# Optimization experiments

Measured on AMD Instinct MI355X. Metric: run time of the kernel, lower is better.

The kernel has to match this reference:

```python
import jax, jax.numpy as jnp
import numpy as np
from jax import lax

B = 1048576
H = 4  # hidden size of both RNN cells


def setup_inputs() -> dict:
    key = jax.random.key(0)
    ks = jax.random.split(key, 16)
    s = 0.3  # small init scale, keeps tanh out of deep saturation
    return {
        "x": jax.random.normal(ks[0], (B, 18), dtype=jnp.float32),
        # r_up = nn.RNNCell(2, 4)
        "Wih_up": jax.random.normal(ks[1], (H, 2), dtype=jnp.float32) * s,
        "Whh_up": jax.random.normal(ks[2], (H, H), dtype=jnp.float32) * s,
        "bih_up": jax.random.normal(ks[3], (H,), dtype=jnp.float32) * s,
        "bhh_up": jax.random.normal(ks[4], (H,), dtype=jnp.float32) * s,
        # fc_obs_1 = nn.Linear(8, 4)
        "W1": jax.random.normal(ks[5], (H, 8), dtype=jnp.float32) * s,
        "b1": jax.random.normal(ks[6], (H,), dtype=jnp.float32) * s,
        # fc_obs_2 = nn.Linear(4, 4)
        "W2": jax.random.normal(ks[7], (H, H), dtype=jnp.float32) * s,
        "b2": jax.random.normal(ks[8], (H,), dtype=jnp.float32) * s,
        # r_down = nn.RNNCell(4, 4)
        "Wih_dn": jax.random.normal(ks[9], (H, H), dtype=jnp.float32) * s,
        "Whh_dn": jax.random.normal(ks[10], (H, H), dtype=jnp.float32) * s,
        "bih_dn": jax.random.normal(ks[11], (H,), dtype=jnp.float32) * s,
        "bhh_dn": jax.random.normal(ks[12], (H,), dtype=jnp.float32) * s,
        # fc_out = nn.Linear(5, 1)
        "Wo": jax.random.normal(ks[13], (1, 5), dtype=jnp.float32) * s,
        "bo": jax.random.normal(ks[14], (1,), dtype=jnp.float32) * s,
    }


def reference(x, Wih_up, Whh_up, bih_up, bhh_up, W1, b1, W2, b2,
              Wih_dn, Whh_dn, bih_dn, bhh_dn, Wo, bo):
    b = x.shape[0]
    obs = x[:, :4]            # [B,4]
    j = x[:, 4:11]            # [B,7] joint angles
    jd = x[:, 11:18]          # [B,7] joint velocities

    # --- upward recurrence: i = 6 .. 0 over joints ---
    seq_up = jnp.stack([j.T, jd.T], axis=-1)[::-1]  # [7,B,2], step order 6..0

    def up_step(h, inp):
        h_new = jnp.tanh(inp @ Wih_up.T + bih_up + h @ Whh_up.T + bhh_up)
        return h_new, h_new

    h_last, h_up_rev = lax.scan(up_step, jnp.zeros((b, H), x.dtype), seq_up)
    h_up = h_up_rev[::-1]  # h_up[i] = hidden after consuming joint i (loop ran 6..0)

    # --- obs MLP ---
    h0 = jnp.tanh(jnp.concatenate([obs, h_last], axis=1) @ W1.T + b1)
    h0 = jnp.tanh(h0 @ W2.T + b2)  # [B,4]

    # --- downward recurrence: i = 0 .. 6, action uses pre-update hidden ---
    def down_step(h, xs):
        hu, ji = xs  # hu: [B,4], ji: [B,1]
        act = jnp.concatenate([h, ji], axis=1) @ Wo.T + bo  # uses h_prev
        h_new = jnp.tanh(hu @ Wih_dn.T + bih_dn + h @ Whh_dn.T + bhh_dn)
        return h_new, act

    _, acts = lax.scan(down_step, h0, (h_up, j.T[:, :, None]))  # acts: [7,B,1]
    return acts[:, :, 0].T  # [B,7]
```

## Files before the change

kernel.cpp:

```cpp
#include <hip/hip_runtime.h>

#define ROWS 256

__device__ __forceinline__ float uni(float v) {
    return __int_as_float(__builtin_amdgcn_readfirstlane(__float_as_int(v)));
}

__device__ __forceinline__ float fast_tanh(float x) {
    float e = __builtin_amdgcn_exp2f(x * 2.885390081777927f);
    float r = __builtin_amdgcn_rcpf(e + 1.0f);
    return fmaf(-2.0f, r, 1.0f);
}

__global__ __launch_bounds__(ROWS)
void recpolicy_kernel(const float* __restrict__ x,
                      const float* __restrict__ Wih_up,
                      const float* __restrict__ Whh_up,
                      const float* __restrict__ bih_up,
                      const float* __restrict__ bhh_up,
                      const float* __restrict__ W1,
                      const float* __restrict__ b1,
                      const float* __restrict__ W2,
                      const float* __restrict__ b2,
                      const float* __restrict__ Wih_dn,
                      const float* __restrict__ Whh_dn,
                      const float* __restrict__ bih_dn,
                      const float* __restrict__ bhh_dn,
                      const float* __restrict__ Wo,
                      const float* __restrict__ bo,
                      float* __restrict__ out)
{
    __shared__ float xs[ROWS * 19];
    const int tid = threadIdx.x;
    const long long row0 = (long long)blockIdx.x * ROWS;

    const float2* xg2 = (const float2*)(x + row0 * 18);
    #pragma unroll
    for (int k = 0; k < 9; ++k) {
        int idx2 = k * ROWS + tid;
        float2 v = xg2[idx2];
        int r = idx2 / 9;
        int c = (idx2 - r * 9) * 2;
        xs[r * 19 + c]     = v.x;
        xs[r * 19 + c + 1] = v.y;
    }

    float wihu[8], whhu[16], bu[4];
    #pragma unroll
    for (int i = 0; i < 8; ++i) wihu[i] = uni(Wih_up[i]);
    #pragma unroll
    for (int i = 0; i < 16; ++i) whhu[i] = uni(Whh_up[i]);
    #pragma unroll
    for (int i = 0; i < 4; ++i) bu[i] = uni(bih_up[i] + bhh_up[i]);

    float w1[32], bb1[4], w2[16], bb2[4];
    #pragma unroll
    for (int i = 0; i < 32; ++i) w1[i] = uni(W1[i]);
    #pragma unroll
    for (int i = 0; i < 4; ++i) bb1[i] = uni(b1[i]);
    #pragma unroll
    for (int i = 0; i < 16; ++i) w2[i] = uni(W2[i]);
    #pragma unroll
    for (int i = 0; i < 4; ++i) bb2[i] = uni(b2[i]);

    float wihd[16], whhd[16], bd[4], wo[5], bO;
    #pragma unroll
    for (int i = 0; i < 16; ++i) wihd[i] = uni(Wih_dn[i]);
    #pragma unroll
    for (int i = 0; i < 16; ++i) whhd[i] = uni(Whh_dn[i]);
    #pragma unroll
    for (int i = 0; i < 4; ++i) bd[i] = uni(bih_dn[i] + bhh_dn[i]);
    #pragma unroll
    for (int i = 0; i < 5; ++i) wo[i] = uni(Wo[i]);
    bO = uni(bo[0]);

    __syncthreads();

    const float* xr = &xs[tid * 19];
    float obs[4], j[7], jd[7];
    #pragma unroll
    for (int i = 0; i < 4; ++i) obs[i] = xr[i];
    #pragma unroll
    for (int i = 0; i < 7; ++i) j[i] = xr[4 + i];
    #pragma unroll
    for (int i = 0; i < 7; ++i) jd[i] = xr[11 + i];

    float h[4] = {0.f, 0.f, 0.f, 0.f};
    float hup[7][4];
    #pragma unroll
    for (int t = 6; t >= 0; --t) {
        float pre[4];
        #pragma unroll
        for (int i = 0; i < 4; ++i) {
            float a = bu[i];
            a = fmaf(j[t],  wihu[i * 2 + 0], a);
            a = fmaf(jd[t], wihu[i * 2 + 1], a);
            #pragma unroll
            for (int k = 0; k < 4; ++k) a = fmaf(h[k], whhu[i * 4 + k], a);
            pre[i] = a;
        }
        #pragma unroll
        for (int i = 0; i < 4; ++i) { h[i] = fast_tanh(pre[i]); hup[t][i] = h[i]; }
    }

    float g[4];
    #pragma unroll
    for (int i = 0; i < 4; ++i) {
        float a = bb1[i];
        #pragma unroll
        for (int k = 0; k < 4; ++k) a = fmaf(obs[k], w1[i * 8 + k], a);
        #pragma unroll
        for (int k = 0; k < 4; ++k) a = fmaf(h[k],   w1[i * 8 + 4 + k], a);
        g[i] = fast_tanh(a);
    }
    #pragma unroll
    for (int i = 0; i < 4; ++i) {
        float a = bb2[i];
        #pragma unroll
        for (int k = 0; k < 4; ++k) a = fmaf(g[k], w2[i * 4 + k], a);
        h[i] = fast_tanh(a);
    }

    float act[7];
    #pragma unroll
    for (int t = 0; t < 7; ++t) {
        float a = bO;
        #pragma unroll
        for (int k = 0; k < 4; ++k) a = fmaf(h[k], wo[k], a);
        a = fmaf(j[t], wo[4], a);
        act[t] = a;
        float pre[4];
        #pragma unroll
        for (int i = 0; i < 4; ++i) {
            float s = bd[i];
            #pragma unroll
            for (int k = 0; k < 4; ++k) s = fmaf(hup[t][k], wihd[i * 4 + k], s);
            #pragma unroll
            for (int k = 0; k < 4; ++k) s = fmaf(h[k],      whhd[i * 4 + k], s);
            pre[i] = s;
        }
        #pragma unroll
        for (int i = 0; i < 4; ++i) h[i] = fast_tanh(pre[i]);
    }

    __syncthreads();
    float* os = xs;
    #pragma unroll
    for (int t = 0; t < 7; ++t) os[tid * 7 + t] = act[t];
    __syncthreads();
    float* og = out + row0 * 7;
    #pragma unroll
    for (int k = 0; k < 7; ++k) og[k * ROWS + tid] = os[k * ROWS + tid];
}

extern "C" void kernel_launch(void* const* d_in, const int* in_sizes, int n_in,
                              void* d_out, int out_size, void* d_ws, size_t ws_size,
                              hipStream_t stream) {
    const float* x      = (const float*)d_in[0];
    const float* Wih_up = (const float*)d_in[1];
    const float* Whh_up = (const float*)d_in[2];
    const float* bih_up = (const float*)d_in[3];
    const float* bhh_up = (const float*)d_in[4];
    const float* W1     = (const float*)d_in[5];
    const float* b1     = (const float*)d_in[6];
    const float* W2     = (const float*)d_in[7];
    const float* b2     = (const float*)d_in[8];
    const float* Wih_dn = (const float*)d_in[9];
    const float* Whh_dn = (const float*)d_in[10];
    const float* bih_dn = (const float*)d_in[11];
    const float* bhh_dn = (const float*)d_in[12];
    const float* Wo     = (const float*)d_in[13];
    const float* bo     = (const float*)d_in[14];
    float* out = (float*)d_out;

    const int Btot = in_sizes[0] / 18;
    const int blocks = Btot / ROWS;

    recpolicy_kernel<<<blocks, ROWS, 0, stream>>>(
        x, Wih_up, Whh_up, bih_up, bhh_up, W1, b1, W2, b2,
        Wih_dn, Whh_dn, bih_dn, bhh_dn, Wo, bo, out);
}
```

Before: 150.4 us.

## Process two rows per thread with packed float2 FMA math

```diff
diff --git a/kernel.cpp b/kernel.cpp
--- a/kernel.cpp
+++ b/kernel.cpp
@@ -1,18 +1,32 @@
 #include <hip/hip_runtime.h>
 
-#define ROWS 256
+#define THREADS 256
+#define RPB 512
+
+typedef float v2f __attribute__((ext_vector_type(2)));
 
 __device__ __forceinline__ float uni(float v) {
     return __int_as_float(__builtin_amdgcn_readfirstlane(__float_as_int(v)));
 }
 
-__device__ __forceinline__ float fast_tanh(float x) {
-    float e = __builtin_amdgcn_exp2f(x * 2.885390081777927f);
-    float r = __builtin_amdgcn_rcpf(e + 1.0f);
-    return fmaf(-2.0f, r, 1.0f);
-}
-
-__global__ __launch_bounds__(ROWS)
+__device__ __forceinline__ v2f vsplat(float s) { v2f r; r.x = s; r.y = s; return r; }
+
+__device__ __forceinline__ v2f vfma2(v2f a, float w, v2f acc) {
+    return __builtin_elementwise_fma(a, vsplat(w), acc);
+}
+
+__device__ __forceinline__ v2f vtanh(v2f x) {
+    v2f xs = x * vsplat(2.885390081777927f);
+    v2f e;
+    e.x = __builtin_amdgcn_exp2f(xs.x);
+    e.y = __builtin_amdgcn_exp2f(xs.y);
+    v2f r;
+    r.x = __builtin_amdgcn_rcpf(e.x + 1.0f);
+    r.y = __builtin_amdgcn_rcpf(e.y + 1.0f);
+    return __builtin_elementwise_fma(vsplat(-2.0f), r, vsplat(1.0f));
+}
+
+__global__ __launch_bounds__(THREADS)
 void recpolicy_kernel(const float* __restrict__ x,
                       const float* __restrict__ Wih_up,
                       const float* __restrict__ Whh_up,
@@ -30,14 +44,14 @@
                       const float* __restrict__ bo,
                       float* __restrict__ out)
 {
-    __shared__ float xs[ROWS * 19];
+    __shared__ float xs[RPB * 19];
     const int tid = threadIdx.x;
-    const long long row0 = (long long)blockIdx.x * ROWS;
+    const long long row0 = (long long)blockIdx.x * RPB;
 
     const float2* xg2 = (const float2*)(x + row0 * 18);
     #pragma unroll
-    for (int k = 0; k < 9; ++k) {
-        int idx2 = k * ROWS + tid;
+    for (int k = 0; k < 18; ++k) {
+        int idx2 = k * THREADS + tid;
         float2 v = xg2[idx2];
         int r = idx2 / 9;
         int c = (idx2 - r * 9) * 2;
@@ -76,81 +90,87 @@
 
     __syncthreads();
 
-    const float* xr = &xs[tid * 19];
-    float obs[4], j[7], jd[7];
-    #pragma unroll
-    for (int i = 0; i < 4; ++i) obs[i] = xr[i];
-    #pragma unroll
-    for (int i = 0; i < 7; ++i) j[i] = xr[4 + i];
-    #pragma unroll
-    for (int i = 0; i < 7; ++i) jd[i] = xr[11 + i];
-
-    float h[4] = {0.f, 0.f, 0.f, 0.f};
-    float hup[7][4];
+    const float* xr0 = &xs[tid * 19];
+    const float* xr1 = &xs[(tid + 256) * 19];
+    v2f obs[4], j[7], jd[7];
+    #pragma unroll
+    for (int i = 0; i < 4; ++i) { obs[i].x = xr0[i];      obs[i].y = xr1[i]; }
+    #pragma unroll
+    for (int i = 0; i < 7; ++i) { j[i].x  = xr0[4 + i];   j[i].y  = xr1[4 + i]; }
+    #pragma unroll
+    for (int i = 0; i < 7; ++i) { jd[i].x = xr0[11 + i];  jd[i].y = xr1[11 + i]; }
+
+    v2f h[4], hup[7][4];
+    #pragma unroll
+    for (int i = 0; i < 4; ++i) h[i] = vsplat(0.0f);
     #pragma unroll
     for (int t = 6; t >= 0; --t) {
-        float pre[4];
+        v2f pre[4];
         #pragma unroll
         for (int i = 0; i < 4; ++i) {
-            float a = bu[i];
-            a = fmaf(j[t],  wihu[i * 2 + 0], a);
-            a = fmaf(jd[t], wihu[i * 2 + 1], a);
+            v2f a = vsplat(bu[i]);
+            a = vfma2(j[t],  wihu[i * 2 + 0], a);
+            a = vfma2(jd[t], wihu[i * 2 + 1], a);
             #pragma unroll
-            for (int k = 0; k < 4; ++k) a = fmaf(h[k], whhu[i * 4 + k], a);
+            for (int k = 0; k < 4; ++k) a = vfma2(h[k], whhu[i * 4 + k], a);
             pre[i] = a;
         }
         #pragma unroll
-        for (int i = 0; i < 4; ++i) { h[i] = fast_tanh(pre[i]); hup[t][i] = h[i]; }
-    }
-
-    float g[4];
+        for (int i = 0; i < 4; ++i) { h[i] = vtanh(pre[i]); hup[t][i] = h[i]; }
+    }
+
+    v2f g[4];
     #pragma unroll
     for (int i = 0; i < 4; ++i) {
-        float a = bb1[i];
-        #pragma unroll
-        for (int k = 0; k < 4; ++k) a = fmaf(obs[k], w1[i * 8 + k], a);
-        #pragma unroll
-        for (int k = 0; k < 4; ++k) a = fmaf(h[k],   w1[i * 8 + 4 + k], a);
-        g[i] = fast_tanh(a);
+        v2f a = vsplat(bb1[i]);
+        #pragma unroll
+        for (int k = 0; k < 4; ++k) a = vfma2(obs[k], w1[i * 8 + k], a);
+        #pragma unroll
+        for (int k = 0; k < 4; ++k) a = vfma2(h[k],   w1[i * 8 + 4 + k], a);
+        g[i] = vtanh(a);
     }
     #pragma unroll
     for (int i = 0; i < 4; ++i) {
-        float a = bb2[i];
-        #pragma unroll
-        for (int k = 0; k < 4; ++k) a = fmaf(g[k], w2[i * 4 + k], a);
-        h[i] = fast_tanh(a);
-    }
-
-    float act[7];
+        v2f a = vsplat(bb2[i]);
+        #pragma unroll
+        for (int k = 0; k < 4; ++k) a = vfma2(g[k], w2[i * 4 + k], a);
+        h[i] = vtanh(a);
+    }
+
+    v2f act[7];
     #pragma unroll
     for (int t = 0; t < 7; ++t) {
-        float a = bO;
-        #pragma unroll
-        for (int k = 0; k < 4; ++k) a = fmaf(h[k], wo[k], a);
-        a = fmaf(j[t], wo[4], a);
+        v2f a = vsplat(bO);
+        #pragma unroll
+        for (int k = 0; k < 4; ++k) a = vfma2(h[k], wo[k], a);
+        a = vfma2(j[t], wo[4], a);
         act[t] = a;
-        float pre[4];
+        v2f pre[4];
         #pragma unroll
         for (int i = 0; i < 4; ++i) {
-            float s = bd[i];
+            v2f s = vsplat(bd[i]);
             #pragma unroll
-            for (int k = 0; k < 4; ++k) s = fmaf(hup[t][k], wihd[i * 4 + k], s);
+            for (int k = 0; k < 4; ++k) s = vfma2(hup[t][k], wihd[i * 4 + k], s);
             #pragma unroll
-            for (int k = 0; k < 4; ++k) s = fmaf(h[k],      whhd[i * 4 + k], s);
+            for (int k = 0; k < 4; ++k) s = vfma2(h[k],      whhd[i * 4 + k], s);
             pre[i] = s;
         }
         #pragma unroll
-        for (int i = 0; i < 4; ++i) h[i] = fast_tanh(pre[i]);
+        for (int i = 0; i < 4; ++i) h[i] = vtanh(pre[i]);
     }
 
     __syncthreads();
     float* os = xs;
     #pragma unroll
-    for (int t = 0; t < 7; ++t) os[tid * 7 + t] = act[t];
+    for (int t = 0; t < 7; ++t) {
+        os[tid * 7 + t]         = act[t].x;
+        os[(tid + 256) * 7 + t] = act[t].y;
+    }
     __syncthreads();
-    float* og = out + row0 * 7;
-    #pragma unroll
-    for (int k = 0; k < 7; ++k) og[k * ROWS + tid] = os[k * ROWS + tid];
+    const float2* os2 = (const float2*)os;
+    float2* og2 = (float2*)(out + row0 * 7);
+    #pragma unroll
+    for (int k = 0; k < 7; ++k) og2[k * THREADS + tid] = os2[k * THREADS + tid];
 }
 
 extern "C" void kernel_launch(void* const* d_in, const int* in_sizes, int n_in,
@@ -174,9 +194,9 @@
     float* out = (float*)d_out;
 
     const int Btot = in_sizes[0] / 18;
-    const int blocks = Btot / ROWS;
-
-    recpolicy_kernel<<<blocks, ROWS, 0, stream>>>(
+    const int blocks = Btot / RPB;
+
+    recpolicy_kernel<<<blocks, THREADS, 0, stream>>>(
         x, Wih_up, Whh_up, bih_up, bhh_up, W1, b1, W2, b2,
         Wih_dn, Whh_dn, bih_dn, bhh_dn, Wo, bo, out);
 }
```

New measurement: 144.0 us. 4.3% less time.
